# Kernel optimization log

Hardware: AMD Instinct MI355X
Metric: run time of the kernel (lower is better)

## Reference

```python
import jax, jax.numpy as jnp
import numpy as np

B, T, F, H, FUT = 64, 512, 64, 512, 96  # batch, past len, features, hidden, future len


def setup_inputs() -> dict:
    key = jax.random.key(0)
    ks = jax.random.split(key, 19)
    s = 1.0 / np.sqrt(H)  # PyTorch LSTM/Linear init scale
    u = lambda k, shape: jax.random.uniform(k, shape, jnp.float32, -s, s)
    inp = {"input_seq": jax.random.normal(ks[0], (B, T, F), jnp.float32)}
    i = 1
    for pre in ("enc", "dec"):
        for l in range(2):
            ins = F if l == 0 else H
            inp[f"{pre}_Wih{l}"] = u(ks[i], (4 * H, ins)); i += 1
            inp[f"{pre}_Whh{l}"] = u(ks[i], (4 * H, H)); i += 1
            inp[f"{pre}_bih{l}"] = u(ks[i], (4 * H,)); i += 1
            inp[f"{pre}_bhh{l}"] = u(ks[i], (4 * H,)); i += 1
    inp["fc_W"] = u(ks[17], (F, H))
    inp["fc_b"] = u(ks[18], (F,))
    return inp


def _cell(x, h, c, Wih, Whh, bih, bhh):
    # PyTorch gate order: i, f, g, o
    g = x @ Wih.T + h @ Whh.T + bih + bhh
    i_, f_, g_, o_ = jnp.split(g, 4, axis=-1)
    c = jax.nn.sigmoid(f_) * c + jax.nn.sigmoid(i_) * jnp.tanh(g_)
    h = jax.nn.sigmoid(o_) * jnp.tanh(c)
    return h, c


def reference(input_seq, enc_Wih0, enc_Whh0, enc_bih0, enc_bhh0,
              enc_Wih1, enc_Whh1, enc_bih1, enc_bhh1,
              dec_Wih0, dec_Whh0, dec_bih0, dec_bhh0,
              dec_Wih1, dec_Whh1, dec_bih1, dec_bhh1,
              fc_W, fc_b):
    b = input_seq.shape[0]
    z = jnp.zeros((b, H), input_seq.dtype)

    def run_layer(x, Wih, Whh, bih, bhh):
        def step(carry, xt):
            h, c = _cell(xt, carry[0], carry[1], Wih, Whh, bih, bhh)
            return (h, c), h
        (h, c), ys = jax.lax.scan(step, (z, z), jnp.swapaxes(x, 0, 1))
        return jnp.swapaxes(ys, 0, 1), h, c

    # encoder (2 layers, eval mode -> no dropout)
    y0, h0, c0 = run_layer(input_seq, enc_Wih0, enc_Whh0, enc_bih0, enc_bhh0)
    _, h1, c1 = run_layer(y0, enc_Wih1, enc_Whh1, enc_bih1, enc_bhh1)

    def dec_step(carry, _):
        x, dh0, dc0, dh1, dc1 = carry
        dh0, dc0 = _cell(x, dh0, dc0, dec_Wih0, dec_Whh0, dec_bih0, dec_bhh0)
        dh1, dc1 = _cell(dh0, dh1, dc1, dec_Wih1, dec_Whh1, dec_bih1, dec_bhh1)
        out = dh1 @ fc_W.T + fc_b
        return (out, dh0, dc0, dh1, dc1), out

    dec_in = input_seq[:, -1, :]
    _, outs = jax.lax.scan(dec_step, (dec_in, h0, c0, h1, c1), None, length=FUT)
    return jnp.swapaxes(outs, 0, 1)  # [B, FUT, F]
```

## Files before the change

### kernel.cpp

```cpp
#include <hip/hip_runtime.h>
#include <stdint.h>

typedef __attribute__((ext_vector_type(8))) short short8;
typedef __attribute__((ext_vector_type(4))) float floatx4;
typedef unsigned short u16;
typedef unsigned int u32;

constexpr int BSZ = 64;
constexpr int SEQT = 512;
constexpr int FIN = 64;
constexpr int HID = 512;
constexpr int NG = 2048;
constexpr int FUTL = 96;
constexpr int K0 = FIN + HID;
constexpr int K1 = HID + HID;
constexpr int K0P = K0 + 8;
constexpr int NGRP = 256;
constexpr int NFCB = 4;
constexpr int NBLK = NGRP + NFCB;
constexpr int NTHR = 256;

constexpr int SLOT_HP = 128 * 256;
constexpr int SLOT_XP = 16 * 256;
constexpr int NSLOT_H = 65;

constexpr size_t S_W0 = (size_t)NG * K0 * 2;
constexpr size_t S_W1 = (size_t)NG * K1 * 2;
constexpr size_t S_FC = (size_t)FIN * HID * 2;

constexpr size_t OFF_WHI_E0 = 0;
constexpr size_t OFF_WLO_E0 = OFF_WHI_E0 + S_W0;
constexpr size_t OFF_WHI_E1 = OFF_WLO_E0 + S_W0;
constexpr size_t OFF_WLO_E1 = OFF_WHI_E1 + S_W1;
constexpr size_t OFF_WHI_D1 = OFF_WLO_E1 + S_W1;
constexpr size_t OFF_WLO_D1 = OFF_WHI_D1 + S_W1;
constexpr size_t OFF_WFH   = OFF_WLO_D1 + S_W1;
constexpr size_t OFF_WFL   = OFF_WFH + S_W1;
constexpr size_t OFF_FCHI  = OFF_WFL + S_W1;
constexpr size_t OFF_FCLO  = OFF_FCHI + S_FC;
constexpr size_t OFF_GX    = OFF_FCLO + S_FC;
constexpr size_t OFF_BEFF  = OFF_GX + (size_t)NG * BSZ * 4;
constexpr size_t OFF_XP    = OFF_BEFF + (size_t)NG * 4;
constexpr size_t OFF_H0P   = OFF_XP + (size_t)SEQT * SLOT_XP * 4;
constexpr size_t OFF_H1P   = OFF_H0P + (size_t)NSLOT_H * SLOT_HP * 4;
constexpr size_t OFF_CNT   = OFF_H1P + (size_t)NSLOT_H * SLOT_HP * 4;
constexpr size_t CNT_BYTES = 65536;

#define FCF(c)   ((c) + 0)
#define PK0(c)   ((c) + 256)
#define PK1(c)   ((c) + 384)
#define GOA0(c)  ((c) + 512)
#define GOA1(c)  ((c) + 2560)

__device__ __forceinline__ u16 f2bf(float f) {
  u32 u = __float_as_uint(f);
  u += 0x7FFFu + ((u >> 16) & 1u);
  return (u16)(u >> 16);
}
__device__ __forceinline__ float bf2f(u16 h) { return __uint_as_float(((u32)h) << 16); }
__device__ __forceinline__ u32 packsplit(float v) {
  u16 h = f2bf(v);
  u16 l = f2bf(v - bf2f(h));
  return (u32)h | ((u32)l << 16);
}

__device__ __forceinline__ float sigf(float x) { return 1.f / (1.f + __expf(-x)); }
__device__ __forceinline__ float tanh_f(float x) {
  float xx = fminf(20.f, fmaxf(-20.f, x));
  float e = __expf(-2.f * xx);
  return (1.f - e) / (1.f + e);
}

__device__ __forceinline__ floatx4 mfma3(short8 ah, short8 al, short8 bh, short8 bl, floatx4 acc) {
  acc = __builtin_amdgcn_mfma_f32_16x16x32_bf16(ah, bh, acc, 0, 0, 0);
  acc = __builtin_amdgcn_mfma_f32_16x16x32_bf16(ah, bl, acc, 0, 0, 0);
  acc = __builtin_amdgcn_mfma_f32_16x16x32_bf16(al, bh, acc, 0, 0, 0);
  return acc;
}

__device__ __forceinline__ void st_sc_u32(u32* p, u32 v) {
  asm volatile("global_store_dword %0, %1, off sc0 sc1" :: "v"(p), "v"(v) : "memory");
}
#define WAITVM0() asm volatile("s_waitcnt vmcnt(0)" ::: "memory")

#define ALD(p) __hip_atomic_load((p), __ATOMIC_RELAXED, __HIP_MEMORY_SCOPE_AGENT)
#define AST(p, v) __hip_atomic_store((p), (v), __ATOMIC_RELAXED, __HIP_MEMORY_SCOPE_AGENT)

__device__ __forceinline__ int slotof(int u) { return u < 0 ? 0 : ((u & 63) + 1); }

__device__ __forceinline__ void ld_frag(const u32* p, short8& ah, short8& al) {
  uint4 a = *(const uint4*)p;
  uint4 b = *(const uint4*)(p + 256);
  union { u32 u[4]; short8 s; } H, L;
  H.u[0] = __builtin_amdgcn_perm(a.y, a.x, 0x05040100u);
  L.u[0] = __builtin_amdgcn_perm(a.y, a.x, 0x07060302u);
  H.u[1] = __builtin_amdgcn_perm(a.w, a.z, 0x05040100u);
  L.u[1] = __builtin_amdgcn_perm(a.w, a.z, 0x07060302u);
  H.u[2] = __builtin_amdgcn_perm(b.y, b.x, 0x05040100u);
  L.u[2] = __builtin_amdgcn_perm(b.y, b.x, 0x07060302u);
  H.u[3] = __builtin_amdgcn_perm(b.w, b.z, 0x05040100u);
  L.u[3] = __builtin_amdgcn_perm(b.w, b.z, 0x07060302u);
  ah = H.s; al = L.s;
}

__global__ void k_split_pair(const float* __restrict__ Wih, const float* __restrict__ Whh,
                             int ins, int K, u16* __restrict__ hi, u16* __restrict__ lo) {
  int n = NG * K;
  for (int idx = blockIdx.x * blockDim.x + threadIdx.x; idx < n; idx += gridDim.x * blockDim.x) {
    int row = idx / K;
    int k = idx - row * K;
    float v = (k < ins) ? Wih[row * ins + k] : Whh[row * HID + (k - ins)];
    u16 h = f2bf(v);
    hi[idx] = h;
    lo[idx] = f2bf(v - bf2f(h));
  }
}

__global__ void k_split_flat(const float* __restrict__ src, u16* __restrict__ hi,
                             u16* __restrict__ lo, int n) {
  for (int idx = blockIdx.x * blockDim.x + threadIdx.x; idx < n; idx += gridDim.x * blockDim.x) {
    float v = src[idx];
    u16 h = f2bf(v);
    hi[idx] = h;
    lo[idx] = f2bf(v - bf2f(h));
  }
}

__global__ void k_fuse(const float* __restrict__ dWih0, const float* __restrict__ dWhh0,
                       const float* __restrict__ fcW,
                       u16* __restrict__ wfh, u16* __restrict__ wfl) {
  __shared__ float wr[FIN];
  const int row = blockIdx.x;
  if (threadIdx.x < FIN) wr[threadIdx.x] = dWih0[row * FIN + threadIdx.x];
  __syncthreads();
  for (int j = threadIdx.x; j < HID; j += blockDim.x) {
    float acc = 0.f;
#pragma unroll
    for (int f = 0; f < FIN; ++f) acc = fmaf(wr[f], fcW[f * HID + j], acc);
    u16 h = f2bf(acc);
    wfh[(size_t)row * K1 + j] = h;
    wfl[(size_t)row * K1 + j] = f2bf(acc - bf2f(h));
    float v2 = dWhh0[row * HID + j];
    u16 h2 = f2bf(v2);
    wfh[(size_t)row * K1 + HID + j] = h2;
    wfl[(size_t)row * K1 + HID + j] = f2bf(v2 - bf2f(h2));
  }
}

__global__ void k_gx(const float* __restrict__ dWih0, const float* __restrict__ in_seq,
                     const float* __restrict__ fcb, const float* __restrict__ bdih0,
                     const float* __restrict__ bdhh0, float* __restrict__ gx,
                     float* __restrict__ beff) {
  __shared__ float xl[BSZ * FIN];
  __shared__ float fb[FIN];
  const int row0 = blockIdx.x * 8;
  for (int i = threadIdx.x; i < BSZ * FIN; i += blockDim.x) {
    int b = i >> 6, f = i & 63;
    xl[i] = in_seq[(b * SEQT + (SEQT - 1)) * FIN + f];
  }
  if (threadIdx.x < FIN) fb[threadIdx.x] = fcb[threadIdx.x];
  __syncthreads();
  for (int i = threadIdx.x; i < 8 * BSZ; i += blockDim.x) {
    int r = row0 + (i >> 6);
    int b = i & 63;
    float acc = 0.f;
#pragma unroll 8
    for (int f = 0; f < FIN; ++f)
      acc = fmaf(dWih0[r * FIN + f], xl[(b << 6) + f] - fb[f], acc);
    gx[r * BSZ + b] = acc;
    if (b == 0) {
      float accb = 0.f;
#pragma unroll 8
      for (int f = 0; f < FIN; ++f) accb = fmaf(dWih0[r * FIN + f], fb[f], accb);
      beff[r] = bdih0[r] + bdhh0[r] + accb;
    }
  }
}

__global__ void k_pack_x(const float* __restrict__ x, u32* __restrict__ xp) {
  int n = BSZ * SEQT * FIN;
  for (int idx = blockIdx.x * blockDim.x + threadIdx.x; idx < n; idx += gridDim.x * blockDim.x) {
    int t = idx / (BSZ * FIN);
    int rem = idx - t * (BSZ * FIN);
    int b = rem >> 6;
    int f = rem & 63;
    u32 pk = packsplit(x[(b * SEQT + t) * FIN + f]);
    int off = ((f >> 2) * 64 + b) * 4 + (f & 3);
    xp[t * SLOT_XP + off] = pk;
  }
}

struct Params {
  const u16 *we0h, *we0l, *we1h, *we1l;
  const u16 *wd1h, *wd1l, *wfh, *wfl;
  const u16 *fch, *fcl;
  const u32 *xp;
  u32 *h0p, *h1p;
  const float *beih0, *behh0, *beih1, *behh1;
  const float *bdih1, *bdhh1;
  const float *gx, *beff;
  const float *fcb;
  float *out;
  u32 *cnt;
};

__device__ __forceinline__ void sweep_pk_c(const u32* pk, u32 target, u32& cache) {
  if (threadIdx.x < 64 && cache < target) {
    u32 a, b;
    do {
      a = ALD(pk + threadIdx.x);
      b = ALD(pk + threadIdx.x + 64);
    } while (!__all(a >= target && b >= target));
    u32 m = a < b ? a : b;
#pragma unroll
    for (int off = 1; off < 64; off <<= 1) {
      u32 o = __shfl_xor(m, off, 64);
      m = o < m ? o : m;
    }
    cache = m;
  }
  __syncthreads();
}

__device__ void sweep_pk_sleep(const u32* pk, u32 target) {
  if (threadIdx.x < 64) {
    while (!__all(ALD(pk + threadIdx.x) >= target && ALD(pk + threadIdx.x + 64) >= target))
      __builtin_amdgcn_s_sleep(1);
  }
  __syncthreads();
}

__device__ __forceinline__ void worker_wait(u32* cell, u32 tok) {
  if (threadIdx.x == 0) {
    while (ALD(cell) < tok) {}
  }
  __syncthreads();
}

__device__ __forceinline__ void fcf_wait_c(u32* fcf, u32 tok, u32& cache) {
  if (threadIdx.x == 0 && cache < tok) {
    u32 m;
    do {
      u32 a = ALD(fcf), b = ALD(fcf + 16), c = ALD(fcf + 32), d = ALD(fcf + 48);
      u32 m1 = a < b ? a : b, m2 = c < d ? c : d;
      m = m1 < m2 ? m1 : m2;
    } while (m < tok);
    cache = m;
  }
  __syncthreads();
}

__device__ __forceinline__ void fence_acq() {
  __builtin_amdgcn_fence(__ATOMIC_ACQUIRE, "agent");
}

__device__ __forceinline__ void arrive(u32* cell, u32 tok) {
  WAITVM0();
  __syncthreads();
  if (threadIdx.x == 0) AST(cell, tok);
}

__device__ void enc_master(const u32* pkOwn, const u32* pkFore, u32* goA, bool farlag) {
  for (int s = 0; s < SEQT; ++s) {
    if (threadIdx.x < 64) {
      int l = threadIdx.x;
      for (;;) {
        bool ok = ALD(pkOwn + l) >= (u32)s && ALD(pkOwn + l + 64) >= (u32)s;
        if (farlag && s >= 63) {
          u32 ft = (u32)(s - 63);
          ok = ok && ALD(pkFore + l) >= ft && ALD(pkFore + l + 64) >= ft;
        }
        if (__all(ok)) break;
      }
    }
    __syncthreads();
    if (threadIdx.x < 128) AST(goA + (threadIdx.x << 4), (u32)(s + 1));
    __syncthreads();
  }
}

template <bool IS_L1>
__device__ void load_w_lds(const u16* __restrict__ gh, const u16* __restrict__ gl,
                           u16* wh, u16* wl, int hc) {
  constexpr int K = IS_L1 ? K1 : K0;
  for (int i = threadIdx.x; i < 16 * K; i += NTHR) {
    int rr, k;
    if (IS_L1) { rr = i >> 10; k = i & 1023; }
    else       { rr = i / K0;  k = i - rr * K0; }
    int gc = ((rr >> 2) * HID) + hc + (rr & 3);
    int dst = IS_L1 ? ((rr << 10) + ((((k >> 3) ^ rr)) << 3) + (k & 7))
                    : (rr * K0P + k);
    wh[dst] = gh[(size_t)gc * K + k];
    wl[dst] = gl[(size_t)gc * K + k];
  }
  __syncthreads();
}

template <bool IS_L1, int KBASE, int LEN>
__device__ __forceinline__ void kpart(const u32* __restrict__ sp,
                                      const u16* __restrict__ wh, const u16* __restrict__ wl,
                                      int r, int quad, int mo, floatx4& acc) {
  const int qo = quad << 3;
  constexpr int NIT = LEN / 32;
  uint4 ra[NIT], rb[NIT];
#pragma unroll
  for (int i = 0; i < NIT; ++i) {
    const u32* p = sp + (((i * 32 + qo) >> 2) << 8) + mo;
    ra[i] = *(const uint4*)p;
    rb[i] = *(const uint4*)(p + 256);
  }
#pragma unroll
  for (int i = 0; i < NIT; ++i) {
    union { u32 u[4]; short8 s; } H, L;
    H.u[0] = __builtin_amdgcn_perm(ra[i].y, ra[i].x, 0x05040100u);
    L.u[0] = __builtin_amdgcn_perm(ra[i].y, ra[i].x, 0x07060302u);
    H.u[1] = __builtin_amdgcn_perm(ra[i].w, ra[i].z, 0x05040100u);
    L.u[1] = __builtin_amdgcn_perm(ra[i].w, ra[i].z, 0x07060302u);
    H.u[2] = __builtin_amdgcn_perm(rb[i].y, rb[i].x, 0x05040100u);
    L.u[2] = __builtin_amdgcn_perm(rb[i].y, rb[i].x, 0x07060302u);
    H.u[3] = __builtin_amdgcn_perm(rb[i].w, rb[i].z, 0x05040100u);
    L.u[3] = __builtin_amdgcn_perm(rb[i].w, rb[i].z, 0x07060302u);
    const int kg = i * 32 + KBASE;
    int woff;
    if (IS_L1) { int c = (kg >> 3) + quad; woff = (r << 10) + ((c ^ r) << 3); }
    else       { woff = r * K0P + kg + qo; }
    short8 bh = *(const short8*)(wh + woff);
    short8 bl = *(const short8*)(wl + woff);
    acc = mfma3(H.s, L.s, bh, bl, acc);
  }
}

__device__ __forceinline__ void epilogue(floatx4 acc, floatx4 bs, float& creg,
                                         u32* __restrict__ oslab,
                                         const float* __restrict__ gxb) {
  const int tid = threadIdx.x, lane = tid & 63;
  const int j = lane & 3;
  const int isel = (lane >> 2) & 3;
  const int slb = lane & 48;
  float gate[4];
#pragma unroll
  for (int q = 0; q < 4; ++q) {
    const int sl = slb + (q << 2) + j;
    float t0 = __shfl(acc[0], sl, 64);
    float t1 = __shfl(acc[1], sl, 64);
    float t2 = __shfl(acc[2], sl, 64);
    float t3 = __shfl(acc[3], sl, 64);
    gate[q] = (isel == 0) ? t0 : (isel == 1) ? t1 : (isel == 2) ? t2 : t3;
  }
  if (gxb != nullptr) {
    const int bb = tid >> 2;
#pragma unroll
    for (int q = 0; q < 4; ++q) gate[q] += gxb[q * (HID * BSZ) + j * BSZ + bb];
  }
  float iv = gate[0] + bs[0];
  float fv = gate[1] + bs[1];
  float gv = gate[2] + bs[2];
  float ov = gate[3] + bs[3];
  float cn = fmaf(sigf(fv), creg, sigf(iv) * tanh_f(gv));
  float hn = sigf(ov) * tanh_f(cn);
  creg = cn;
  st_sc_u32(oslab + tid, packsplit(hn));
}

__device__ void fc_step(int t, int blkq, const u32* __restrict__ h1slot,
                        const u16* __restrict__ fh, const u16* __restrict__ fl,
                        const float* __restrict__ fcb, float* __restrict__ out) {
  const int tid = threadIdx.x, lane = tid & 63, w = tid >> 6;
  const int quad = lane >> 4, r = lane & 15;
  const int m = (w << 4) + r;
  const int qo = quad << 3;
  const int mo = m << 2;
  const int col = (blkq << 4) + r;
  floatx4 acc = {0.f, 0.f, 0.f, 0.f};
#pragma unroll
  for (int kk = 0; kk < HID; kk += 32) {
    short8 ah, al;
    ld_frag(h1slot + (((kk + qo) >> 2) << 8) + mo, ah, al);
    short8 b1 = *(const short8*)(fh + col * HID + kk + qo);
    short8 b2 = *(const short8*)(fl + col * HID + kk + qo);
    acc = mfma3(ah, al, b1, b2, acc);
  }
  float bias = fcb[col];
#pragma unroll
  for (int i = 0; i < 4; ++i) {
    int b = (w << 4) + (quad << 2) + i;
    out[(b * FUTL + t) * FIN + col] = acc[i] + bias;
  }
}

__global__ __launch_bounds__(NTHR, 1) void lstm_coop(Params p) {
  __shared__ u16 wsmem[32768];
  u16* wh = wsmem;
  u16* wl = wsmem + 16 * 1024;
  const int blk = blockIdx.x;
  const int tid = threadIdx.x;

  u32* fcf = FCF(p.cnt);
  u32* pk0 = PK0(p.cnt);
  u32* pk1 = PK1(p.cnt);

  if (blk >= NGRP) {
    const int fi = blk - NGRP;
    if (fi == 0) enc_master(pk0, pk1, GOA0(p.cnt), true);
    if (fi == 1) enc_master(pk1, pk0, GOA1(p.cnt), false);
    for (int t = 0; t < FUTL; ++t) {
      sweep_pk_sleep(pk1, (u32)(513 + t));
      if ((t & 63) == 0) fence_acq();
      fc_step(t, fi, p.h1p + (size_t)slotof(512 + t) * SLOT_HP,
              p.fch, p.fcl, p.fcb, p.out);
      WAITVM0();
      __syncthreads();
      if (tid == 0) AST(fcf + fi * 16, (u32)(t + 1));
    }
    return;
  }

  const int grp = blk >> 7;
  const int lidx = blk & 127;
  const int hc = lidx << 2;
  const int lane = tid & 63, w = tid >> 6;
  const int quad = lane >> 4, r = lane & 15;
  const int mo = ((w << 4) + r) << 2;

  u32* myGoA = (grp ? GOA1(p.cnt) : GOA0(p.cnt)) + lidx * 16;
  u32* myPk  = (grp ? pk1 : pk0) + lidx;

  floatx4 bse, bsd;
  {
    int ch = hc + (tid & 3);
    const float* bi  = grp ? p.beih1 : p.beih0;
    const float* bh2 = grp ? p.behh1 : p.behh0;
#pragma unroll
    for (int q = 0; q < 4; ++q) {
      bse[q] = bi[q * HID + ch] + bh2[q * HID + ch];
      bsd[q] = grp ? (p.bdih1[q * HID + ch] + p.bdhh1[q * HID + ch])
                   : p.beff[q * HID + ch];
    }
  }
  float creg = 0.f;

  if (!grp) {
    u32 cpk0 = 0, cpk1 = 0;
    load_w_lds<false>(p.we0h, p.we0l, wh, wl, hc);
    for (int s = 0; s < SEQT; ++s) {
      floatx4 acc = {0.f, 0.f, 0.f, 0.f};
      kpart<false, 0, FIN>(p.xp + (size_t)s * SLOT_XP, wh, wl, r, quad, mo, acc);
      worker_wait(myGoA, (u32)(s + 1));
      if ((s & 63) == 0 && s) fence_acq();
      kpart<false, FIN, HID>(p.h0p + (size_t)slotof(s - 1) * SLOT_HP, wh, wl, r, quad, mo, acc);
      epilogue(acc, bse, creg,
               p.h0p + (size_t)slotof(s) * SLOT_HP + (lidx << 8), nullptr);
      arrive(myPk, (u32)(s + 1));
    }
    load_w_lds<true>(p.wfh, p.wfl, wh, wl, hc);
    for (int t = 0; t < FUTL; ++t) {
      floatx4 acc = {0.f, 0.f, 0.f, 0.f};
      sweep_pk_c(pk0, (u32)(512 + t), cpk0);
      if (t == 0) sweep_pk_c(pk1, 449u, cpk1);
      if ((t & 63) == 0) fence_acq();
      kpart<true, 512, HID>(p.h0p + (size_t)slotof(511 + t) * SLOT_HP, wh, wl, r, quad, mo, acc);
      if (t) {
        sweep_pk_c(pk1, (u32)(512 + t), cpk1);
        kpart<true, 0, HID>(p.h1p + (size_t)slotof(511 + t) * SLOT_HP, wh, wl, r, quad, mo, acc);
      }
      epilogue(acc, bsd, creg,
               p.h0p + (size_t)slotof(512 + t) * SLOT_HP + (lidx << 8),
               (t == 0) ? (p.gx + hc * BSZ) : nullptr);
      arrive(myPk, (u32)(513 + t));
    }
  } else {
    u32 cpk0 = 0, cfc = 0;
    load_w_lds<true>(p.we1h, p.we1l, wh, wl, hc);
    for (int t = 0; t < SEQT; ++t) {
      floatx4 acc = {0.f, 0.f, 0.f, 0.f};
      sweep_pk_c(pk0, (u32)(t + 1), cpk0);
      if ((t & 63) == 0 && t) fence_acq();
      kpart<true, 0, HID>(p.h0p + (size_t)slotof(t) * SLOT_HP, wh, wl, r, quad, mo, acc);
      worker_wait(myGoA, (u32)(t + 1));
      kpart<true, 512, HID>(p.h1p + (size_t)slotof(t - 1) * SLOT_HP, wh, wl, r, quad, mo, acc);
      epilogue(acc, bse, creg,
               p.h1p + (size_t)slotof(t) * SLOT_HP + (lidx << 8), nullptr);
      arrive(myPk, (u32)(t + 1));
    }
    u32 cpk1own = 0;
    load_w_lds<true>(p.wd1h, p.wd1l, wh, wl, hc);
    for (int t = 0; t < FUTL; ++t) {
      floatx4 acc = {0.f, 0.f, 0.f, 0.f};
      sweep_pk_c(pk1, (u32)(512 + t), cpk1own);
      if (t >= 64 && (t & 15) == 0) fcf_wait_c(fcf, (u32)(t - 48), cfc);
      if ((t & 63) == 0) fence_acq();
      kpart<true, 512, HID>(p.h1p + (size_t)slotof(511 + t) * SLOT_HP, wh, wl, r, quad, mo, acc);
      sweep_pk_c(pk0, (u32)(513 + t), cpk0);
      kpart<true, 0, HID>(p.h0p + (size_t)slotof(512 + t) * SLOT_HP, wh, wl, r, quad, mo, acc);
      epilogue(acc, bsd, creg,
               p.h1p + (size_t)slotof(512 + t) * SLOT_HP + (lidx << 8), nullptr);
      arrive(myPk, (u32)(513 + t));
    }
  }
}

extern "C" void kernel_launch(void* const* d_in, const int* in_sizes, int n_in,
                              void* d_out, int out_size, void* d_ws, size_t ws_size,
                              hipStream_t stream) {
  (void)in_sizes; (void)n_in; (void)out_size; (void)ws_size;
  const float* in_seq = (const float*)d_in[0];
  const float* eWih0 = (const float*)d_in[1];
  const float* eWhh0 = (const float*)d_in[2];
  const float* ebih0 = (const float*)d_in[3];
  const float* ebhh0 = (const float*)d_in[4];
  const float* eWih1 = (const float*)d_in[5];
  const float* eWhh1 = (const float*)d_in[6];
  const float* ebih1 = (const float*)d_in[7];
  const float* ebhh1 = (const float*)d_in[8];
  const float* dWih0 = (const float*)d_in[9];
  const float* dWhh0 = (const float*)d_in[10];
  const float* dbih0 = (const float*)d_in[11];
  const float* dbhh0 = (const float*)d_in[12];
  const float* dWih1 = (const float*)d_in[13];
  const float* dWhh1 = (const float*)d_in[14];
  const float* dbih1 = (const float*)d_in[15];
  const float* dbhh1 = (const float*)d_in[16];
  const float* fcW  = (const float*)d_in[17];
  const float* fcb  = (const float*)d_in[18];

  char* ws = (char*)d_ws;
  u16* we0h = (u16*)(ws + OFF_WHI_E0); u16* we0l = (u16*)(ws + OFF_WLO_E0);
  u16* we1h = (u16*)(ws + OFF_WHI_E1); u16* we1l = (u16*)(ws + OFF_WLO_E1);
  u16* wd1h = (u16*)(ws + OFF_WHI_D1); u16* wd1l = (u16*)(ws + OFF_WLO_D1);
  u16* wfh  = (u16*)(ws + OFF_WFH);    u16* wfl  = (u16*)(ws + OFF_WFL);
  u16* fch  = (u16*)(ws + OFF_FCHI);   u16* fcl  = (u16*)(ws + OFF_FCLO);
  float* gx   = (float*)(ws + OFF_GX);
  float* beff = (float*)(ws + OFF_BEFF);
  u32* xp   = (u32*)(ws + OFF_XP);
  u32* h0p  = (u32*)(ws + OFF_H0P);
  u32* h1p  = (u32*)(ws + OFF_H1P);
  u32* cnt  = (u32*)(ws + OFF_CNT);

  hipMemsetAsync(ws + OFF_H0P, 0, (size_t)SLOT_HP * 4, stream);
  hipMemsetAsync(ws + OFF_H1P, 0, (size_t)SLOT_HP * 4, stream);
  hipMemsetAsync(ws + OFF_CNT, 0, CNT_BYTES, stream);

  k_split_pair<<<512, 256, 0, stream>>>(eWih0, eWhh0, FIN, K0, we0h, we0l);
  k_split_pair<<<512, 256, 0, stream>>>(eWih1, eWhh1, HID, K1, we1h, we1l);
  k_split_pair<<<512, 256, 0, stream>>>(dWih1, dWhh1, HID, K1, wd1h, wd1l);
  k_split_flat<<<128, 256, 0, stream>>>(fcW, fch, fcl, FIN * HID);
  k_fuse<<<NG, 256, 0, stream>>>(dWih0, dWhh0, fcW, wfh, wfl);
  k_gx<<<256, 256, 0, stream>>>(dWih0, in_seq, fcb, dbih0, dbhh0, gx, beff);
  k_pack_x<<<1024, 256, 0, stream>>>(in_seq, xp);

  Params p;
  p.we0h = we0h; p.we0l = we0l; p.we1h = we1h; p.we1l = we1l;
  p.wd1h = wd1h; p.wd1l = wd1l; p.wfh = wfh; p.wfl = wfl;
  p.fch = fch; p.fcl = fcl;
  p.xp = xp; p.h0p = h0p; p.h1p = h1p;
  p.beih0 = ebih0; p.behh0 = ebhh0; p.beih1 = ebih1; p.behh1 = ebhh1;
  p.bdih1 = dbih1; p.bdhh1 = dbhh1;
  p.gx = gx; p.beff = beff;
  p.fcb = fcb;
  p.out = (float*)d_out;
  p.cnt = cnt;

  lstm_coop<<<dim3(NBLK), dim3(NTHR), 0, stream>>>(p);
}
```

Before: 4.019 ms.

## Replace master-block go signals with decentralized per-worker done-flag sweeps

Removes the two encoder master blocks that relayed go tokens to each worker, so every worker now polls its group's per-block done counters directly. The done counters are padded to one per 64-byte stride, which avoids false sharing between arrivals. This takes a relay hop off the per-timestep critical path of the recurrent chain. In exchange, 128 blocks each sweep 128 flags every step, which raises polling traffic on shared cache lines, and the FC-side wait condition is retuned.

```diff
diff --git a/kernel.cpp b/kernel.cpp
--- a/kernel.cpp
+++ b/kernel.cpp
@@ -47,10 +47,8 @@
 constexpr size_t CNT_BYTES = 65536;
 
 #define FCF(c)   ((c) + 0)
-#define PK0(c)   ((c) + 256)
-#define PK1(c)   ((c) + 384)
-#define GOA0(c)  ((c) + 512)
-#define GOA1(c)  ((c) + 2560)
+#define DONE0(c) ((c) + 256)
+#define DONE1(c) ((c) + 2304)
 
 __device__ __forceinline__ u16 f2bf(float f) {
   u32 u = __float_as_uint(f);
@@ -204,35 +202,39 @@
   u32 *cnt;
 };
 
-__device__ __forceinline__ void sweep_pk_c(const u32* pk, u32 target, u32& cache) {
-  if (threadIdx.x < 64 && cache < target) {
-    u32 a, b;
-    do {
-      a = ALD(pk + threadIdx.x);
-      b = ALD(pk + threadIdx.x + 64);
-    } while (!__all(a >= target && b >= target));
-    u32 m = a < b ? a : b;
-#pragma unroll
-    for (int off = 1; off < 64; off <<= 1) {
-      u32 o = __shfl_xor(m, off, 64);
-      m = o < m ? o : m;
-    }
-    cache = m;
-  }
-  __syncthreads();
-}
-
-__device__ void sweep_pk_sleep(const u32* pk, u32 target) {
+__device__ __forceinline__ void sweep_hot(u32* arr, u32 T) {
   if (threadIdx.x < 64) {
-    while (!__all(ALD(pk + threadIdx.x) >= target && ALD(pk + threadIdx.x + 64) >= target))
+    int l = threadIdx.x;
+    while (!__all(ALD(arr + l * 16) >= T && ALD(arr + (l + 64) * 16) >= T))
       __builtin_amdgcn_s_sleep(1);
   }
   __syncthreads();
 }
 
-__device__ __forceinline__ void worker_wait(u32* cell, u32 tok) {
-  if (threadIdx.x == 0) {
-    while (ALD(cell) < tok) {}
+__device__ __forceinline__ void sweep_min_c(u32* arr, u32 T, u32& cache, volatile u32* sbc) {
+  if (cache < T) {
+    if (threadIdx.x < 64) {
+      u32 a, b;
+      do {
+        a = ALD(arr + threadIdx.x * 16);
+        b = ALD(arr + (threadIdx.x + 64) * 16);
+      } while (!__all(a >= T && b >= T));
+      u32 m = a < b ? a : b;
+#pragma unroll
+      for (int o = 1; o < 64; o <<= 1) { u32 x = __shfl_xor(m, o, 64); m = x < m ? x : m; }
+      if (threadIdx.x == 0) *sbc = m;
+    }
+    __syncthreads();
+    cache = *sbc;
+    __syncthreads();
+  }
+}
+
+__device__ void fc_sweep(u32* arr, u32 T) {
+  if (threadIdx.x < 64) {
+    int l = threadIdx.x;
+    while (!__all(ALD(arr + l * 16) >= T && ALD(arr + (l + 64) * 16) >= T))
+      __builtin_amdgcn_s_sleep(16);
   }
   __syncthreads();
 }
@@ -258,25 +260,6 @@
   WAITVM0();
   __syncthreads();
   if (threadIdx.x == 0) AST(cell, tok);
-}
-
-__device__ void enc_master(const u32* pkOwn, const u32* pkFore, u32* goA, bool farlag) {
-  for (int s = 0; s < SEQT; ++s) {
-    if (threadIdx.x < 64) {
-      int l = threadIdx.x;
-      for (;;) {
-        bool ok = ALD(pkOwn + l) >= (u32)s && ALD(pkOwn + l + 64) >= (u32)s;
-        if (farlag && s >= 63) {
-          u32 ft = (u32)(s - 63);
-          ok = ok && ALD(pkFore + l) >= ft && ALD(pkFore + l + 64) >= ft;
-        }
-        if (__all(ok)) break;
-      }
-    }
-    __syncthreads();
-    if (threadIdx.x < 128) AST(goA + (threadIdx.x << 4), (u32)(s + 1));
-    __syncthreads();
-  }
 }
 
 template <bool IS_L1>
@@ -390,21 +373,24 @@
 
 __global__ __launch_bounds__(NTHR, 1) void lstm_coop(Params p) {
   __shared__ u16 wsmem[32768];
+  __shared__ u32 sbc;
   u16* wh = wsmem;
   u16* wl = wsmem + 16 * 1024;
   const int blk = blockIdx.x;
   const int tid = threadIdx.x;
 
   u32* fcf = FCF(p.cnt);
-  u32* pk0 = PK0(p.cnt);
-  u32* pk1 = PK1(p.cnt);
+  u32* d0 = DONE0(p.cnt);
+  u32* d1 = DONE1(p.cnt);
 
   if (blk >= NGRP) {
     const int fi = blk - NGRP;
-    if (fi == 0) enc_master(pk0, pk1, GOA0(p.cnt), true);
-    if (fi == 1) enc_master(pk1, pk0, GOA1(p.cnt), false);
+    if (tid == 0) {
+      while (ALD(d1) < 513u) __builtin_amdgcn_s_sleep(127);
+    }
+    __syncthreads();
     for (int t = 0; t < FUTL; ++t) {
-      sweep_pk_sleep(pk1, (u32)(513 + t));
+      fc_sweep(d1, (u32)(513 + t));
       if ((t & 63) == 0) fence_acq();
       fc_step(t, fi, p.h1p + (size_t)slotof(512 + t) * SLOT_HP,
               p.fch, p.fcl, p.fcb, p.out);
@@ -422,8 +408,7 @@
   const int quad = lane >> 4, r = lane & 15;
   const int mo = ((w << 4) + r) << 2;
 
-  u32* myGoA = (grp ? GOA1(p.cnt) : GOA0(p.cnt)) + lidx * 16;
-  u32* myPk  = (grp ? pk1 : pk0) + lidx;
+  u32* myDone = (grp ? d1 : d0) + lidx * 16;
 
   floatx4 bse, bsd;
   {
@@ -440,61 +425,62 @@
   float creg = 0.f;
 
   if (!grp) {
-    u32 cpk0 = 0, cpk1 = 0;
+    u32 d1min = 0;
     load_w_lds<false>(p.we0h, p.we0l, wh, wl, hc);
     for (int s = 0; s < SEQT; ++s) {
       floatx4 acc = {0.f, 0.f, 0.f, 0.f};
       kpart<false, 0, FIN>(p.xp + (size_t)s * SLOT_XP, wh, wl, r, quad, mo, acc);
-      worker_wait(myGoA, (u32)(s + 1));
+      if (s >= 63) sweep_min_c(d1, (u32)(s - 63), d1min, &sbc);
+      sweep_hot(d0, (u32)s);
       if ((s & 63) == 0 && s) fence_acq();
       kpart<false, FIN, HID>(p.h0p + (size_t)slotof(s - 1) * SLOT_HP, wh, wl, r, quad, mo, acc);
       epilogue(acc, bse, creg,
                p.h0p + (size_t)slotof(s) * SLOT_HP + (lidx << 8), nullptr);
-      arrive(myPk, (u32)(s + 1));
+      arrive(myDone, (u32)(s + 1));
     }
     load_w_lds<true>(p.wfh, p.wfl, wh, wl, hc);
     for (int t = 0; t < FUTL; ++t) {
       floatx4 acc = {0.f, 0.f, 0.f, 0.f};
-      sweep_pk_c(pk0, (u32)(512 + t), cpk0);
-      if (t == 0) sweep_pk_c(pk1, 449u, cpk1);
+      sweep_hot(d0, (u32)(512 + t));
+      if (t == 0) sweep_min_c(d1, 449u, d1min, &sbc);
       if ((t & 63) == 0) fence_acq();
       kpart<true, 512, HID>(p.h0p + (size_t)slotof(511 + t) * SLOT_HP, wh, wl, r, quad, mo, acc);
       if (t) {
-        sweep_pk_c(pk1, (u32)(512 + t), cpk1);
+        sweep_hot(d1, (u32)(512 + t));
         kpart<true, 0, HID>(p.h1p + (size_t)slotof(511 + t) * SLOT_HP, wh, wl, r, quad, mo, acc);
       }
       epilogue(acc, bsd, creg,
                p.h0p + (size_t)slotof(512 + t) * SLOT_HP + (lidx << 8),
                (t == 0) ? (p.gx + hc * BSZ) : nullptr);
-      arrive(myPk, (u32)(513 + t));
+      arrive(myDone, (u32)(513 + t));
     }
   } else {
-    u32 cpk0 = 0, cfc = 0;
+    u32 d0min = 0;
+    u32 fcseen = 0;
     load_w_lds<true>(p.we1h, p.we1l, wh, wl, hc);
     for (int t = 0; t < SEQT; ++t) {
       floatx4 acc = {0.f, 0.f, 0.f, 0.f};
-      sweep_pk_c(pk0, (u32)(t + 1), cpk0);
+      sweep_min_c(d0, (u32)(t + 1), d0min, &sbc);
       if ((t & 63) == 0 && t) fence_acq();
       kpart<true, 0, HID>(p.h0p + (size_t)slotof(t) * SLOT_HP, wh, wl, r, quad, mo, acc);
-      worker_wait(myGoA, (u32)(t + 1));
+      sweep_hot(d1, (u32)t);
       kpart<true, 512, HID>(p.h1p + (size_t)slotof(t - 1) * SLOT_HP, wh, wl, r, quad, mo, acc);
       epilogue(acc, bse, creg,
                p.h1p + (size_t)slotof(t) * SLOT_HP + (lidx << 8), nullptr);
-      arrive(myPk, (u32)(t + 1));
-    }
-    u32 cpk1own = 0;
+      arrive(myDone, (u32)(t + 1));
+    }
     load_w_lds<true>(p.wd1h, p.wd1l, wh, wl, hc);
     for (int t = 0; t < FUTL; ++t) {
       floatx4 acc = {0.f, 0.f, 0.f, 0.f};
-      sweep_pk_c(pk1, (u32)(512 + t), cpk1own);
-      if (t >= 64 && (t & 15) == 0) fcf_wait_c(fcf, (u32)(t - 48), cfc);
+      sweep_hot(d1, (u32)(512 + t));
+      if (t >= 64) fcf_wait_c(fcf, (u32)(t - 63), fcseen);
       if ((t & 63) == 0) fence_acq();
       kpart<true, 512, HID>(p.h1p + (size_t)slotof(511 + t) * SLOT_HP, wh, wl, r, quad, mo, acc);
-      sweep_pk_c(pk0, (u32)(513 + t), cpk0);
+      sweep_hot(d0, (u32)(513 + t));
       kpart<true, 0, HID>(p.h0p + (size_t)slotof(512 + t) * SLOT_HP, wh, wl, r, quad, mo, acc);
       epilogue(acc, bsd, creg,
                p.h1p + (size_t)slotof(512 + t) * SLOT_HP + (lidx << 8), nullptr);
-      arrive(myPk, (u32)(513 + t));
+      arrive(myDone, (u32)(513 + t));
     }
   }
 }
```

After: 3.489 ms. 1.15x faster.
